# Optimization experiments

Hardware: AMD Instinct MI355X
Metric: run time of the kernel (lower is better)

Reference implementation:

```python
import jax, jax.numpy as jnp
import numpy as np

D_MODEL = 1024


def setup_inputs() -> dict:
    key = jax.random.key(0)
    ks = jax.random.split(key, 8)
    B, S, D = 32, 2048, D_MODEL
    scale = 1.0 / np.sqrt(D)
    return {
        "query": jax.random.normal(ks[0], (B, D), dtype=jnp.float32),
        "keys": jax.random.normal(ks[1], (B, S, D), dtype=jnp.float32),
        "Wq_w": jax.random.normal(ks[2], (D, D), dtype=jnp.float32) * scale,
        "Wq_b": jax.random.normal(ks[3], (D,), dtype=jnp.float32) * 0.01,
        "Wk_w": jax.random.normal(ks[4], (D, D), dtype=jnp.float32) * scale,
        "Wk_b": jax.random.normal(ks[5], (D,), dtype=jnp.float32) * 0.01,
        "v_w": jax.random.normal(ks[6], (D,), dtype=jnp.float32) * scale,
        "v_b": jax.random.normal(ks[7], (1,), dtype=jnp.float32) * 0.01,
    }


def reference(query, keys, Wq_w, Wq_b, Wk_w, Wk_b, v_w, v_b):
    # q: [B, 1, D], k: [B, S, D]
    q = (query @ Wq_w.T + Wq_b)[:, None, :]
    k = keys @ Wk_w.T + Wk_b
    # additive (Bahdanau) scores: [B, S]
    scores = jnp.einsum("bsd,d->bs", jnp.tanh(q + k), v_w) + v_b[0]
    attn = jax.nn.softmax(scores, axis=-1)
    # weighted sum over original keys: [B, D]
    context = jnp.einsum("bs,bsd->bd", attn, keys)
    return (context, attn)
```

## Files before the change

kernel.cpp:

```cpp
#include <hip/hip_runtime.h>
#include <cstddef>
#include <cstdint>

#define BATCH 32
#define SEQ 2048
#define DM 1024

typedef __attribute__((ext_vector_type(8))) _Float16 half8v;
typedef __attribute__((ext_vector_type(4))) _Float16 half4v;
typedef __attribute__((ext_vector_type(4))) float f32x4;

__device__ _Float16 g_Bpk[8 * 32 * 4 * 128 * 8];
__device__ float g_q[BATCH * DM];
__device__ float g_sp[16][BATCH * SEQ];

__device__ __forceinline__ float tanh_fast(float x) {
    float e = __expf(2.0f * x);
    return 1.0f - 2.0f / (e + 1.0f);
}

__device__ __forceinline__ void gload16(const void* g, void* l) {
    __builtin_amdgcn_global_load_lds((__attribute__((address_space(1))) void*)g,
                                     (__attribute__((address_space(3))) void*)l, 16, 0, 0);
}

__global__ __launch_bounds__(256) void packb_kernel(const float* __restrict__ Wk_w) {
    int p = blockIdx.x;
    int nc = p >> 5, kt = p & 31;
    int t = threadIdx.x;
    int row = t >> 1, hh = t & 1;
    const float* src = Wk_w + (size_t)(nc * 128 + row) * DM + kt * 32;
#pragma unroll
    for (int i = 0; i < 2; ++i) {
        int kc = hh * 2 + i;
        float4 w0 = *reinterpret_cast<const float4*>(src + kc * 8);
        float4 w1 = *reinterpret_cast<const float4*>(src + kc * 8 + 4);
        union { _Float16 f[8]; half8v v; } h;
        h.f[0] = (_Float16)w0.x; h.f[1] = (_Float16)w0.y;
        h.f[2] = (_Float16)w0.z; h.f[3] = (_Float16)w0.w;
        h.f[4] = (_Float16)w1.x; h.f[5] = (_Float16)w1.y;
        h.f[6] = (_Float16)w1.z; h.f[7] = (_Float16)w1.w;
        *reinterpret_cast<half8v*>(
            &g_Bpk[((((size_t)p) * 4 + kc) * 128 + row) * 8]) = h.v;
    }
}

__global__ __launch_bounds__(256) void init_kernel(float* __restrict__ context) {
    int idx = blockIdx.x * 256 + threadIdx.x;
    if (idx < BATCH * DM) context[idx] = 0.f;
}

__global__ __launch_bounds__(256) void qproj_kernel(const float* __restrict__ query,
                                                    const float* __restrict__ Wq_w,
                                                    const float* __restrict__ Wq_b) {
    int d = blockIdx.x;
    int t = threadIdx.x;
    __shared__ float wrow[DM];
    __shared__ float part[8][32];
    reinterpret_cast<float4*>(wrow)[t] =
        reinterpret_cast<const float4*>(Wq_w + (size_t)d * DM)[t];
    __syncthreads();
    int b = t & 31, seg = t >> 5;
    const float4* qp = reinterpret_cast<const float4*>(query + b * DM + seg * 128);
    const float4* wp = reinterpret_cast<const float4*>(wrow + seg * 128);
    float acc = 0.f;
#pragma unroll
    for (int i = 0; i < 32; ++i) {
        float4 qv = qp[i];
        float4 wv = wp[i];
        acc += qv.x * wv.x + qv.y * wv.y + qv.z * wv.z + qv.w * wv.w;
    }
    part[seg][b] = acc;
    __syncthreads();
    if (t < 32) {
        float s = Wq_b[d];
#pragma unroll
        for (int g = 0; g < 8; ++g) s += part[g][t];
        g_q[t * DM + d] = s;
    }
}

#define BM 128
#define BN 128
#define BK 32
#define NT (DM / BK)

__global__ __launch_bounds__(256, 3) void scores_kernel(const float* __restrict__ keys,
                                                        const float* __restrict__ Wk_b,
                                                        const float* __restrict__ v_w) {
    __shared__ _Float16 AhS[2][4][BM + 1][8];
    __shared__ _Float16 BhS[2][4][BN + 1][8];

    const unsigned bid = blockIdx.x;
    const unsigned L = (bid & 7u) * 512u + (bid >> 3);
    const int mtile = (int)(L >> 3);
    const int nchunk = (int)(L & 7u);
    const int m0 = mtile * BM;
    const int n0 = nchunk * BN;
    const int b = m0 >> 11;

    const int t = threadIdx.x;
    const int w = t >> 6, l = t & 63;
    const int wm = w >> 1, wn = w & 1;
    const int lr = l & 15, lg = l >> 4;

    const int acol = (l & 7) * 4;
    const int akc = (l & 7) >> 1;
    const int aoff = ((l & 7) & 1) * 4;
    const float* Ap = keys + (size_t)(m0 + w * 32 + (l >> 3)) * DM + acol;

    const _Float16* Bp = g_Bpk + ((((size_t)nchunk * 32) * 4 + w) * 128 + l) * 8;

    float4 as[4];

    f32x4 acc[4][4];
#pragma unroll
    for (int mi = 0; mi < 4; ++mi)
#pragma unroll
        for (int ni = 0; ni < 4; ++ni)
#pragma unroll
            for (int c = 0; c < 4; ++c) acc[mi][ni][c] = 0.f;

#define LOAD_A(kt)                                                               \
    {                                                                            \
        _Pragma("unroll") for (int j = 0; j < 4; ++j)                            \
            as[j] = *reinterpret_cast<const float4*>(                            \
                Ap + (size_t)j * 8 * DM + (kt) * BK);                            \
    }
#define ISSUE_B(kt, bufi)                                                        \
    {                                                                            \
        const _Float16* gb = Bp + (size_t)(kt) * (4 * 128 * 8);                  \
        _Pragma("unroll") for (int rg = 0; rg < 2; ++rg)                         \
            gload16(gb + rg * 512, &BhS[bufi][w][rg * 64][0]);                   \
    }
#define STAGE_A(bufi)                                                            \
    {                                                                            \
        _Pragma("unroll") for (int j = 0; j < 4; ++j) {                          \
            const float* fa = reinterpret_cast<const float*>(&as[j]);            \
            union { _Float16 f[4]; half4v v; } h;                                \
            h.f[0] = (_Float16)fa[0]; h.f[1] = (_Float16)fa[1];                  \
            h.f[2] = (_Float16)fa[2]; h.f[3] = (_Float16)fa[3];                  \
            *reinterpret_cast<half4v*>(                                          \
                &AhS[bufi][akc][w * 32 + j * 8 + (l >> 3)][aoff]) = h.v;         \
        }                                                                        \
    }
#define COMPUTE(bufi)                                                            \
    {                                                                            \
        half8v bhv[4];                                                           \
        _Pragma("unroll") for (int ni = 0; ni < 4; ++ni)                         \
            bhv[ni] = *reinterpret_cast<const half8v*>(                          \
                &BhS[bufi][lg][wn * 64 + ni * 16 + lr][0]);                      \
        __builtin_amdgcn_s_setprio(1);                                           \
        _Pragma("unroll") for (int mi = 0; mi < 4; ++mi) {                       \
            half8v ahv = *reinterpret_cast<const half8v*>(                       \
                &AhS[bufi][lg][wm * 64 + mi * 16 + lr][0]);                      \
            _Pragma("unroll") for (int ni = 0; ni < 4; ++ni)                     \
                acc[mi][ni] = __builtin_amdgcn_mfma_f32_16x16x32_f16(            \
                    ahv, bhv[ni], acc[mi][ni], 0, 0, 0);                         \
        }                                                                        \
        __builtin_amdgcn_s_setprio(0);                                          \
    }

    LOAD_A(0);
    ISSUE_B(0, 0);
    STAGE_A(0);
    LOAD_A(1);
    __syncthreads();

    int cur = 0;
    for (int tt = 0; tt < NT; ++tt) {
        if (tt + 1 < NT) ISSUE_B(tt + 1, cur ^ 1);
        COMPUTE(cur);
        if (tt + 1 < NT) STAGE_A(cur ^ 1);
        if (tt + 2 < NT) LOAD_A(tt + 2);
        __syncthreads();
        cur ^= 1;
    }

    float qb[4], vw[4];
#pragma unroll
    for (int ni = 0; ni < 4; ++ni) {
        int n = n0 + wn * 64 + ni * 16 + lr;
        qb[ni] = g_q[b * DM + n] + Wk_b[n];
        vw[ni] = v_w[n];
    }
#pragma unroll
    for (int mi = 0; mi < 4; ++mi) {
#pragma unroll
        for (int rg = 0; rg < 4; ++rg) {
            float p = 0.f;
#pragma unroll
            for (int ni = 0; ni < 4; ++ni) {
                float val = acc[mi][ni][rg] + qb[ni];
                p += tanh_fast(val) * vw[ni];
            }
#pragma unroll
            for (int off = 8; off >= 1; off >>= 1) p += __shfl_xor(p, off, 16);
            if (lr == 0)
                g_sp[nchunk * 2 + wn][m0 + wm * 64 + mi * 16 + lg * 4 + rg] = p;
        }
    }
#undef LOAD_A
#undef ISSUE_B
#undef STAGE_A
#undef COMPUTE
}

__global__ __launch_bounds__(256) void softmax_kernel(float* __restrict__ attn) {
    int b = blockIdx.x;
    int tid = threadIdx.x;
    __shared__ float redm[4];
    __shared__ float reds[4];
    float v[8];
    float mx = -1e30f;
#pragma unroll
    for (int i = 0; i < 8; ++i) {
        int idx = b * SEQ + i * 256 + tid;
        float s = 0.f;
#pragma unroll
        for (int pslot = 0; pslot < 16; ++pslot) s += g_sp[pslot][idx];
        v[i] = s;
        mx = fmaxf(mx, v[i]);
    }
#pragma unroll
    for (int off = 32; off >= 1; off >>= 1) mx = fmaxf(mx, __shfl_xor(mx, off));
    int wid = tid >> 6;
    if ((tid & 63) == 0) redm[wid] = mx;
    __syncthreads();
    mx = fmaxf(fmaxf(redm[0], redm[1]), fmaxf(redm[2], redm[3]));
    float sum = 0.f;
#pragma unroll
    for (int i = 0; i < 8; ++i) {
        v[i] = expf(v[i] - mx);
        sum += v[i];
    }
#pragma unroll
    for (int off = 32; off >= 1; off >>= 1) sum += __shfl_xor(sum, off);
    if ((tid & 63) == 0) reds[wid] = sum;
    __syncthreads();
    sum = reds[0] + reds[1] + reds[2] + reds[3];
    float inv = 1.f / sum;
#pragma unroll
    for (int i = 0; i < 8; ++i) attn[b * SEQ + i * 256 + tid] = v[i] * inv;
}

__global__ __launch_bounds__(256) void context_kernel(const float* __restrict__ keys,
                                                      const float* __restrict__ attn,
                                                      float* __restrict__ context) {
    int id = blockIdx.x;
    int schunk = id & 15;
    int b = id >> 4;
    int tid = threadIdx.x;
    __shared__ float a_s[128];
    if (tid < 128) a_s[tid] = attn[b * SEQ + schunk * 128 + tid];
    __syncthreads();
    const float4* kp =
        reinterpret_cast<const float4*>(keys + ((size_t)b * SEQ + schunk * 128) * DM) + tid;
    float4 acc = {0.f, 0.f, 0.f, 0.f};
#pragma unroll 4
    for (int s = 0; s < 128; ++s) {
        float4 kv = kp[(size_t)s * (DM / 4)];
        float a = a_s[s];
        acc.x += a * kv.x; acc.y += a * kv.y; acc.z += a * kv.z; acc.w += a * kv.w;
    }
    atomicAdd(&context[b * DM + tid * 4 + 0], acc.x);
    atomicAdd(&context[b * DM + tid * 4 + 1], acc.y);
    atomicAdd(&context[b * DM + tid * 4 + 2], acc.z);
    atomicAdd(&context[b * DM + tid * 4 + 3], acc.w);
}

extern "C" void kernel_launch(void* const* d_in, const int* in_sizes, int n_in,
                              void* d_out, int out_size, void* d_ws, size_t ws_size,
                              hipStream_t stream) {
    const float* query = (const float*)d_in[0];
    const float* keys  = (const float*)d_in[1];
    const float* Wq_w  = (const float*)d_in[2];
    const float* Wq_b  = (const float*)d_in[3];
    const float* Wk_w  = (const float*)d_in[4];
    const float* Wk_b  = (const float*)d_in[5];
    const float* v_w   = (const float*)d_in[6];

    float* context = (float*)d_out;
    float* attn    = context + BATCH * DM;

    hipLaunchKernelGGL(packb_kernel, dim3(256), dim3(256), 0, stream, Wk_w);
    hipLaunchKernelGGL(init_kernel, dim3(128), dim3(256), 0, stream, context);
    hipLaunchKernelGGL(qproj_kernel, dim3(DM), dim3(256), 0, stream, query, Wq_w, Wq_b);
    hipLaunchKernelGGL(scores_kernel, dim3((BATCH * SEQ / BM) * (DM / BN)), dim3(256), 0, stream,
                       keys, Wk_b, v_w);
    hipLaunchKernelGGL(softmax_kernel, dim3(BATCH), dim3(256), 0, stream, attn);
    hipLaunchKernelGGL(context_kernel, dim3(512), dim3(256), 0, stream, keys, attn, context);
}
```

Baseline: 286.1 us.

## Load packed B fragments straight into registers instead of staging through LDS

Repacks Wk into a fragment-major fp16 layout so each lane can read its MFMA B operand directly from global memory (cached in L2) into registers. The B tile no longer goes through LDS via global_load_lds, and the main loop is unrolled by two with register double-buffering of the B fragments. This cuts LDS traffic and LDS footprint, which may allow higher occupancy. In exchange, each wave issues redundant global loads for B (the two wm waves sharing a wn column read the same data), and register pressure rises.

```diff
diff --git a/kernel.cpp b/kernel.cpp
--- a/kernel.cpp
+++ b/kernel.cpp
@@ -10,7 +10,7 @@
 typedef __attribute__((ext_vector_type(4))) _Float16 half4v;
 typedef __attribute__((ext_vector_type(4))) float f32x4;
 
-__device__ _Float16 g_Bpk[8 * 32 * 4 * 128 * 8];
+__device__ _Float16 g_Bpk[8 * 8 * 32 * 4 * 16 * 8];
 __device__ float g_q[BATCH * DM];
 __device__ float g_sp[16][BATCH * SEQ];
 
@@ -19,29 +19,24 @@
     return 1.0f - 2.0f / (e + 1.0f);
 }
 
-__device__ __forceinline__ void gload16(const void* g, void* l) {
-    __builtin_amdgcn_global_load_lds((__attribute__((address_space(1))) void*)g,
-                                     (__attribute__((address_space(3))) void*)l, 16, 0, 0);
-}
-
 __global__ __launch_bounds__(256) void packb_kernel(const float* __restrict__ Wk_w) {
-    int p = blockIdx.x;
-    int nc = p >> 5, kt = p & 31;
+    int blk = blockIdx.x;
+    int nc = blk >> 3, sub = blk & 7;
     int t = threadIdx.x;
-    int row = t >> 1, hh = t & 1;
-    const float* src = Wk_w + (size_t)(nc * 128 + row) * DM + kt * 32;
-#pragma unroll
-    for (int i = 0; i < 2; ++i) {
-        int kc = hh * 2 + i;
-        float4 w0 = *reinterpret_cast<const float4*>(src + kc * 8);
-        float4 w1 = *reinterpret_cast<const float4*>(src + kc * 8 + 4);
+    int row = t & 15, kgrp = (t >> 4) & 3, kt0 = t >> 6;
+    const float* src = Wk_w + (size_t)(nc * 128 + sub * 16 + row) * DM;
+    _Float16* dst = g_Bpk + (size_t)blk * 16384;
+#pragma unroll
+    for (int pass = 0; pass < 8; ++pass) {
+        int kt = pass * 4 + kt0;
+        float4 w0 = *reinterpret_cast<const float4*>(src + kt * 32 + kgrp * 8);
+        float4 w1 = *reinterpret_cast<const float4*>(src + kt * 32 + kgrp * 8 + 4);
         union { _Float16 f[8]; half8v v; } h;
         h.f[0] = (_Float16)w0.x; h.f[1] = (_Float16)w0.y;
         h.f[2] = (_Float16)w0.z; h.f[3] = (_Float16)w0.w;
         h.f[4] = (_Float16)w1.x; h.f[5] = (_Float16)w1.y;
         h.f[6] = (_Float16)w1.z; h.f[7] = (_Float16)w1.w;
-        *reinterpret_cast<half8v*>(
-            &g_Bpk[((((size_t)p) * 4 + kc) * 128 + row) * 8]) = h.v;
+        *reinterpret_cast<half8v*>(&dst[(size_t)((kt * 4 + kgrp) * 16 + row) * 8]) = h.v;
     }
 }
 
@@ -89,7 +84,6 @@
                                                         const float* __restrict__ Wk_b,
                                                         const float* __restrict__ v_w) {
     __shared__ _Float16 AhS[2][4][BM + 1][8];
-    __shared__ _Float16 BhS[2][4][BN + 1][8];
 
     const unsigned bid = blockIdx.x;
     const unsigned L = (bid & 7u) * 512u + (bid >> 3);
@@ -104,14 +98,15 @@
     const int wm = w >> 1, wn = w & 1;
     const int lr = l & 15, lg = l >> 4;
 
-    const int acol = (l & 7) * 4;
     const int akc = (l & 7) >> 1;
     const int aoff = ((l & 7) & 1) * 4;
-    const float* Ap = keys + (size_t)(m0 + w * 32 + (l >> 3)) * DM + acol;
-
-    const _Float16* Bp = g_Bpk + ((((size_t)nchunk * 32) * 4 + w) * 128 + l) * 8;
+    const float* Ap = keys + (size_t)(m0 + w * 32 + (l >> 3)) * DM + (l & 7) * 4;
+
+    const _Float16* Bp = g_Bpk + ((size_t)(nchunk * 8 + wn * 4)) * 16384
+                               + (size_t)(l >> 4) * 128 + (size_t)(l & 15) * 8;
 
     float4 as[4];
+    half8v bE[4], bO[4];
 
     f32x4 acc[4][4];
 #pragma unroll
@@ -127,11 +122,11 @@
             as[j] = *reinterpret_cast<const float4*>(                            \
                 Ap + (size_t)j * 8 * DM + (kt) * BK);                            \
     }
-#define ISSUE_B(kt, bufi)                                                        \
-    {                                                                            \
-        const _Float16* gb = Bp + (size_t)(kt) * (4 * 128 * 8);                  \
-        _Pragma("unroll") for (int rg = 0; rg < 2; ++rg)                         \
-            gload16(gb + rg * 512, &BhS[bufi][w][rg * 64][0]);                   \
+#define LOAD_BF(kt, dst)                                                         \
+    {                                                                            \
+        _Pragma("unroll") for (int ni = 0; ni < 4; ++ni)                         \
+            dst[ni] = *reinterpret_cast<const half8v*>(                          \
+                Bp + (size_t)ni * 16384 + (size_t)(kt) * 512);                   \
     }
 #define STAGE_A(bufi)                                                            \
     {                                                                            \
@@ -144,37 +139,37 @@
                 &AhS[bufi][akc][w * 32 + j * 8 + (l >> 3)][aoff]) = h.v;         \
         }                                                                        \
     }
-#define COMPUTE(bufi)                                                            \
-    {                                                                            \
-        half8v bhv[4];                                                           \
-        _Pragma("unroll") for (int ni = 0; ni < 4; ++ni)                         \
-            bhv[ni] = *reinterpret_cast<const half8v*>(                          \
-                &BhS[bufi][lg][wn * 64 + ni * 16 + lr][0]);                      \
+#define COMPUTE(bufi, breg)                                                      \
+    {                                                                            \
         __builtin_amdgcn_s_setprio(1);                                           \
         _Pragma("unroll") for (int mi = 0; mi < 4; ++mi) {                       \
             half8v ahv = *reinterpret_cast<const half8v*>(                       \
                 &AhS[bufi][lg][wm * 64 + mi * 16 + lr][0]);                      \
             _Pragma("unroll") for (int ni = 0; ni < 4; ++ni)                     \
                 acc[mi][ni] = __builtin_amdgcn_mfma_f32_16x16x32_f16(            \
-                    ahv, bhv[ni], acc[mi][ni], 0, 0, 0);                         \
+                    ahv, breg[ni], acc[mi][ni], 0, 0, 0);                        \
         }                                                                        \
         __builtin_amdgcn_s_setprio(0);                                          \
     }
 
     LOAD_A(0);
-    ISSUE_B(0, 0);
     STAGE_A(0);
     LOAD_A(1);
-    __syncthreads();
-
-    int cur = 0;
-    for (int tt = 0; tt < NT; ++tt) {
-        if (tt + 1 < NT) ISSUE_B(tt + 1, cur ^ 1);
-        COMPUTE(cur);
-        if (tt + 1 < NT) STAGE_A(cur ^ 1);
+    LOAD_BF(0, bE);
+    __syncthreads();
+
+    for (int tt = 0; tt + 1 < NT; tt += 2) {
+        LOAD_BF(tt + 1, bO);
+        COMPUTE(0, bE);
+        STAGE_A(1);
         if (tt + 2 < NT) LOAD_A(tt + 2);
         __syncthreads();
-        cur ^= 1;
+
+        if (tt + 2 < NT) LOAD_BF(tt + 2, bE);
+        COMPUTE(1, bO);
+        if (tt + 2 < NT) STAGE_A(0);
+        if (tt + 3 < NT) LOAD_A(tt + 3);
+        __syncthreads();
     }
 
     float qb[4], vw[4];
@@ -201,7 +196,7 @@
         }
     }
 #undef LOAD_A
-#undef ISSUE_B
+#undef LOAD_BF
 #undef STAGE_A
 #undef COMPUTE
 }
@@ -283,7 +278,7 @@
     float* context = (float*)d_out;
     float* attn    = context + BATCH * DM;
 
-    hipLaunchKernelGGL(packb_kernel, dim3(256), dim3(256), 0, stream, Wk_w);
+    hipLaunchKernelGGL(packb_kernel, dim3(64), dim3(256), 0, stream, Wk_w);
     hipLaunchKernelGGL(init_kernel, dim3(128), dim3(256), 0, stream, context);
     hipLaunchKernelGGL(qproj_kernel, dim3(DM), dim3(256), 0, stream, query, Wq_w, Wq_b);
     hipLaunchKernelGGL(scores_kernel, dim3((BATCH * SEQ / BM) * (DM / BN)), dim3(256), 0, stream,
```

Measured after the change: 271.7 us. -5.0%, faster.
